# Kernel optimization log

Measured on AMD Instinct MI355X. Metric: run time of the kernel, lower is better.

Reference implementation:

```python
import jax, jax.numpy as jnp
import numpy as np

N0, N1, N2 = 200_000, 100_000, 80_000
F = 32
K5, K3 = 125, 27
M1, M2, M3, M4 = 20_000, 20_000, 30_000, 20_000
EPS = 1e-5


def sparse_conv(feats, W, in_idx, out_idx, n_out):
    """Gather-GEMM-scatter sparse conv. feats:[Nin,Cin], W:[K,Cin,Cout],
    in_idx/out_idx:[K,M] kernel map. Returns [n_out, Cout]."""
    g = feats[in_idx]                                  # [K, M, Cin] gather
    contrib = jnp.einsum('kmc,kcd->kmd', g, W)         # per-offset GEMM
    cout = W.shape[-1]
    out = jnp.zeros((n_out, cout), feats.dtype)
    return out.at[out_idx.reshape(-1)].add(contrib.reshape(-1, cout))


def bn(x, g, b):
    m = x.mean(0)
    v = x.var(0)
    return (x - m) * jax.lax.rsqrt(v + EPS) * g + b


def setup_inputs():
    key = jax.random.key(0)
    ks = jax.random.split(key, 16)
    W_SCALE = 0.02
    inp = {
        'x_feats': jax.random.normal(ks[0], (N0, 1), jnp.float32),
        'w1a': jax.random.normal(ks[1], (K5, 1, F), jnp.float32) * W_SCALE,
        'w1b': jax.random.normal(ks[2], (K5, F, F), jnp.float32) * W_SCALE,
        'w1c': jax.random.normal(ks[3], (K5, F, F), jnp.float32) * W_SCALE,
        'w2': jax.random.normal(ks[4], (K3, F, 2 * F), jnp.float32) * W_SCALE,
        'w3a': jax.random.normal(ks[5], (K3, 2 * F, 4 * F), jnp.float32) * W_SCALE,
        'w3b': jax.random.normal(ks[6], (K3, 4 * F, 8 * F), jnp.float32) * W_SCALE,
        'bn1b_g': jnp.ones((F,), jnp.float32), 'bn1b_b': jnp.zeros((F,), jnp.float32),
        'bn1c_g': jnp.ones((F,), jnp.float32), 'bn1c_b': jnp.zeros((F,), jnp.float32),
        'bn3a_g': jnp.ones((4 * F,), jnp.float32), 'bn3a_b': jnp.zeros((4 * F,), jnp.float32),
        'bn3b_g': jnp.ones((8 * F,), jnp.float32), 'bn3b_b': jnp.zeros((8 * F,), jnp.float32),
        'km1a_in': jax.random.randint(ks[7], (K5, M1), 0, N0, jnp.int32),
        'km1a_out': jax.random.randint(ks[8], (K5, M1), 0, N1, jnp.int32),
        'km1b_in': jax.random.randint(ks[9], (K5, M2), 0, N1, jnp.int32),
        'km1b_out': jax.random.randint(ks[10], (K5, M2), 0, N1, jnp.int32),
        'km1c_in': jax.random.randint(ks[11], (K5, M2), 0, N1, jnp.int32),
        'km1c_out': jax.random.randint(ks[12], (K5, M2), 0, N1, jnp.int32),
        'km2_in': jax.random.randint(ks[13], (K3, M3), 0, N1, jnp.int32),
        'km2_out': jax.random.randint(ks[14], (K3, M3), 0, N2, jnp.int32),
        'km3a_in': jax.random.randint(jax.random.fold_in(key, 20), (K3, M4), 0, N2, jnp.int32),
        'km3a_out': jax.random.randint(jax.random.fold_in(key, 21), (K3, M4), 0, N2, jnp.int32),
        'km3b_in': jax.random.randint(jax.random.fold_in(key, 22), (K3, M4), 0, N2, jnp.int32),
        'km3b_out': jax.random.randint(jax.random.fold_in(key, 23), (K3, M4), 0, N2, jnp.int32),
        'n1': N1,
        'n2': N2,
    }
    return inp


def reference(x_feats, w1a, w1b, w1c, w2, w3a, w3b,
              bn1b_g, bn1b_b, bn1c_g, bn1c_b, bn3a_g, bn3a_b, bn3b_g, bn3b_b,
              km1a_in, km1a_out, km1b_in, km1b_out, km1c_in, km1c_out,
              km2_in, km2_out, km3a_in, km3a_out, km3b_in, km3b_out, n1, n2):
    # enc1: conv(1->F, k5, s2) + ReLU
    h = jax.nn.relu(sparse_conv(x_feats, w1a, km1a_in, km1a_out, n1))
    # conv(F->F, k5) + BN + ReLU
    h = jax.nn.relu(bn(sparse_conv(h, w1b, km1b_in, km1b_out, n1), bn1b_g, bn1b_b))
    # conv(F->F, k5) + BN + ReLU
    x_e1 = jax.nn.relu(bn(sparse_conv(h, w1c, km1c_in, km1c_out, n1), bn1c_g, bn1c_b))
    # conv2: conv(F->2F, k3) onto c_out coordinates (no activation)
    h2 = sparse_conv(x_e1, w2, km2_in, km2_out, n2)
    # enc2: conv(2F->4F, k3) + BN + ReLU
    h2 = jax.nn.relu(bn(sparse_conv(h2, w3a, km3a_in, km3a_out, n2), bn3a_g, bn3a_b))
    # conv(4F->8F, k3) + BN + ReLU
    x_e2 = jax.nn.relu(bn(sparse_conv(h2, w3b, km3b_in, km3b_out, n2), bn3b_g, bn3b_b))
    return (x_e1, x_e2)
```

## Files before the change

### kernel.cpp

```cpp
#include <hip/hip_runtime.h>
#include <hip/hip_fp16.h>
#include <cstdint>
#include <algorithm>

#define N1c 100000
#define N2c 80000
#define EPSc 1e-5f
#define STRIDE_N1 102400
#define STRIDE_N2 81920

typedef _Float16 fp16x8 __attribute__((ext_vector_type(8)));
typedef float f32x4 __attribute__((ext_vector_type(4)));

__global__ __launch_bounds__(256) void rank2d_kernel(
    const int* __restrict__ out_idx, int* __restrict__ rank,
    int* __restrict__ bins, int E, int M, int q, int stride)
{
    for (int e = blockIdx.x * 256 + threadIdx.x; e < E; e += gridDim.x * 256) {
        int chunk = (e / M) / q;
        rank[e] = atomicAdd(&bins[chunk * stride + out_idx[e]], 1);
    }
}

__global__ __launch_bounds__(256) void scan1(
    const int* __restrict__ bins, int* __restrict__ ptr,
    int* __restrict__ bsums, int n)
{
    __shared__ int lds[256];
    int base = blockIdx.x * 1024;
    int v[4]; int t = 0;
    #pragma unroll
    for (int i = 0; i < 4; ++i) {
        int idx = base + threadIdx.x * 4 + i;
        v[i] = idx < n ? bins[idx] : 0;
        t += v[i];
    }
    lds[threadIdx.x] = t; __syncthreads();
    for (int off = 1; off < 256; off <<= 1) {
        int x = threadIdx.x >= off ? lds[threadIdx.x - off] : 0;
        __syncthreads();
        lds[threadIdx.x] += x;
        __syncthreads();
    }
    int run = lds[threadIdx.x] - t;
    if (threadIdx.x == 255) bsums[blockIdx.x] = lds[255];
    #pragma unroll
    for (int i = 0; i < 4; ++i) {
        int idx = base + threadIdx.x * 4 + i;
        if (idx < n) ptr[idx] = run;
        run += v[i];
    }
}

__global__ __launch_bounds__(64) void scan2s(
    int* __restrict__ bsums, int bpc, int nch)
{
    int c = threadIdx.x;
    if (c < nch) {
        int run = 0;
        for (int i = 0; i < bpc; ++i) {
            int idx = c * bpc + i;
            int t = bsums[idx]; bsums[idx] = run; run += t;
        }
    }
}

__global__ __launch_bounds__(256) void scan3(
    int* __restrict__ ptr, const int* __restrict__ bsums, int n)
{
    int idx = blockIdx.x * 1024 + threadIdx.x * 4;
    int add = bsums[blockIdx.x];
    #pragma unroll
    for (int i = 0; i < 4; ++i)
        if (idx + i < n) ptr[idx + i] += add;
}

__global__ __launch_bounds__(256) void scatter_1a(
    const float* __restrict__ x, const int* __restrict__ iin,
    const int* __restrict__ iout, const int* __restrict__ ptr,
    const int* __restrict__ rank, float2* __restrict__ payload, int E, int M)
{
    for (int e = blockIdx.x * 256 + threadIdx.x; e < E; e += gridDim.x * 256) {
        int k = e / M;
        float2 p; p.x = x[iin[e]]; p.y = __int_as_float(k);
        payload[ptr[iout[e]] + rank[e]] = p;
    }
}

__global__ __launch_bounds__(256) void phaseB_1a(
    const float2* __restrict__ payload, const int* __restrict__ ptr,
    const float* __restrict__ W, float* __restrict__ out, int n)
{
    __shared__ float Wl[125 * 32];
    for (int i = threadIdx.x; i < 125 * 32; i += 256) Wl[i] = W[i];
    __syncthreads();
    int total = n * 32;
    for (int idx = blockIdx.x * 256 + threadIdx.x; idx < total; idx += gridDim.x * 256) {
        int o = idx >> 5, c = idx & 31;
        int s0 = ptr[o], s1 = ptr[o + 1];
        float acc = 0.f;
        for (int s = s0; s < s1; ++s) {
            float2 p = payload[s];
            acc = fmaf(p.x, Wl[(__float_as_int(p.y) << 5) + c], acc);
        }
        out[idx] = fmaxf(acc, 0.f);
    }
}

template <int CIN, int CTILE, int WST, int GMODE>
__global__ __launch_bounds__(256) void phaseA_mfma(
    const float* __restrict__ feats, const float* __restrict__ W,
    const int* __restrict__ in_idx, const int* __restrict__ out_idx,
    const int* __restrict__ ptr, const int* __restrict__ rank,
    __half* __restrict__ contrib, int M,
    const float* __restrict__ sc, const float* __restrict__ sh)
{
    constexpr int PP  = 128;
    constexpr int NK  = CIN / 32;
    constexpr int NCF = CTILE / 16;
    constexpr int NRF = 2;
    constexpr int GCHK = (CIN * 2) / 16;
    constexpr int GSM  = (GCHK < 8 ? GCHK : 8) - 1;
    static_assert(CIN % 32 == 0 && CTILE % 16 == 0, "");

    __shared__ __align__(16) _Float16 Gl[PP * CIN];
    __shared__ __align__(16) _Float16 Wt[CTILE * CIN];
    __shared__ int sslot[PP];

    const int tid  = threadIdx.x;
    const int wave = tid >> 6;
    const int lane = tid & 63;
    const int k    = blockIdx.y;

    const int* iin  = in_idx  + (size_t)k * M;
    const int* iout = out_idx + (size_t)k * M;
    const int* rk   = rank    + (size_t)k * M;
    const float* Wk = W + (size_t)k * CIN * WST;

    for (int base = blockIdx.x * PP; base < M; base += gridDim.x * PP) {
        if (tid < PP && base + tid < M)
            sslot[tid] = ptr[iout[base + tid]] + rk[base + tid];

        {
            int r  = tid & (PP - 1);
            int hh = tid >> 7;
            int p  = base + r;
            if (p < M) {
                const int c0 = hh * (CIN / 2);
                const float* fr = feats + (size_t)iin[p] * CIN + c0;
                #pragma unroll
                for (int c = 0; c < CIN / 2; c += 8) {
                    float a[8];
                    *(float4*)&a[0] = *(const float4*)(fr + c);
                    *(float4*)&a[4] = *(const float4*)(fr + c + 4);
                    if (GMODE == 2) {
                        float s[8], h[8];
                        *(float4*)&s[0] = *(const float4*)(sc + c0 + c);
                        *(float4*)&s[4] = *(const float4*)(sc + c0 + c + 4);
                        *(float4*)&h[0] = *(const float4*)(sh + c0 + c);
                        *(float4*)&h[4] = *(const float4*)(sh + c0 + c + 4);
                        #pragma unroll
                        for (int j = 0; j < 8; ++j)
                            a[j] = fmaxf(fmaf(a[j], s[j], h[j]), 0.f);
                    }
                    _Float16 t[8];
                    #pragma unroll
                    for (int j = 0; j < 8; ++j) t[j] = (_Float16)a[j];
                    int col = c0 + c;
                    int idx = r * CIN + ((((col >> 3) ^ (r & GSM))) << 3);
                    *(uint4*)&Gl[idx] = *(uint4*)t;
                }
            }
        }

        for (int i = tid; i < (CTILE / 4) * (CIN / 4); i += 256) {
            int c4 = (i % (CTILE / 4)) * 4;
            int k4 = (i / (CTILE / 4)) * 4;
            const float* wr = Wk + (size_t)k4 * WST + c4;
            float a0[4], a1[4], a2[4], a3[4];
            *(float4*)a0 = *(const float4*)wr;
            *(float4*)a1 = *(const float4*)(wr + WST);
            *(float4*)a2 = *(const float4*)(wr + 2 * (size_t)WST);
            *(float4*)a3 = *(const float4*)(wr + 3 * (size_t)WST);
            #pragma unroll
            for (int j = 0; j < 4; ++j) {
                _Float16 t[4] = { (_Float16)a0[j], (_Float16)a1[j],
                                  (_Float16)a2[j], (_Float16)a3[j] };
                int row = c4 + j;
                int idx = row * CIN + (((k4 >> 3) ^ (row & GSM)) << 3) + (k4 & 7);
                *(uint2*)&Wt[idx] = *(uint2*)t;
            }
        }
        __syncthreads();

        f32x4 acc[NRF][NCF];
        #pragma unroll
        for (int rf = 0; rf < NRF; ++rf)
            #pragma unroll
            for (int cf = 0; cf < NCF; ++cf)
                acc[rf][cf] = (f32x4){0.f, 0.f, 0.f, 0.f};

        const int lrow = lane & 15;
        const int lk8  = (lane >> 4) * 8;
        const int p0   = wave * 32;
        #pragma unroll
        for (int kk = 0; kk < NK; ++kk) {
            int col = kk * 32 + lk8;
            fp16x8 afr[NRF];
            #pragma unroll
            for (int rf = 0; rf < NRF; ++rf) {
                int r = p0 + rf * 16 + lrow;
                afr[rf] = *(const fp16x8*)
                    &Gl[r * CIN + (((col >> 3) ^ (r & GSM)) << 3)];
            }
            #pragma unroll
            for (int cf = 0; cf < NCF; ++cf) {
                int r = cf * 16 + lrow;
                fp16x8 bfr = *(const fp16x8*)
                    &Wt[r * CIN + (((col >> 3) ^ (r & GSM)) << 3)];
                #pragma unroll
                for (int rf = 0; rf < NRF; ++rf)
                    acc[rf][cf] = __builtin_amdgcn_mfma_f32_16x16x32_f16(
                        afr[rf], bfr, acc[rf][cf], 0, 0, 0);
            }
        }

        #pragma unroll
        for (int rf = 0; rf < NRF; ++rf) {
            int prb = p0 + rf * 16 + (lane >> 4) * 4;
            #pragma unroll
            for (int b = 0; b < 4; ++b) {
                int pr = prb + b;
                if (base + pr < M) {
                    size_t s = (size_t)sslot[pr];
                    #pragma unroll
                    for (int cf = 0; cf < NCF; ++cf)
                        contrib[s * CTILE + cf * 16 + lrow] =
                            __float2half(acc[rf][cf][b]);
                }
            }
        }
        __syncthreads();
    }
}

template <int CSTR, bool STATS>
__global__ __launch_bounds__(256) void phaseB8(
    const __half* __restrict__ contrib, const int* __restrict__ ptr,
    float* __restrict__ out, int n, int ostr, int accum,
    double* __restrict__ statsbuf, int sqoff)
{
    float s1 = 0.f, s2 = 0.f;
    int total = n * CSTR;
    for (int idx = blockIdx.x * 256 + threadIdx.x; idx < total; idx += gridDim.x * 256) {
        int o = idx / CSTR, c = idx % CSTR;
        int a = ptr[o], b = ptr[o + 1];
        float acc = accum ? out[(size_t)o * ostr + c] : 0.f;
        for (int s = a; s < b; ++s)
            acc += __half2float(contrib[(size_t)s * CSTR + c]);
        out[(size_t)o * ostr + c] = acc;
        if (STATS) { s1 += acc; s2 += acc * acc; }
    }
    if constexpr (STATS) {
        __shared__ double l1[256], l2[256];
        l1[threadIdx.x] = (double)s1; l2[threadIdx.x] = (double)s2;
        __syncthreads();
        for (int off = 128; off >= CSTR; off >>= 1) {
            if (threadIdx.x < (unsigned)off) {
                l1[threadIdx.x] += l1[threadIdx.x + off];
                l2[threadIdx.x] += l2[threadIdx.x + off];
            }
            __syncthreads();
        }
        if (threadIdx.x < CSTR) {
            atomicAdd(&statsbuf[threadIdx.x], l1[threadIdx.x]);
            atomicAdd(&statsbuf[sqoff + threadIdx.x], l2[threadIdx.x]);
        }
    }
}

template <int C>
__global__ __launch_bounds__(256) void make_scsh(
    const double* __restrict__ sums, const float* __restrict__ g,
    const float* __restrict__ b, float* __restrict__ sc, float* __restrict__ sh,
    double inv_n)
{
    int c = threadIdx.x;
    if (c < C) {
        double mean = sums[c] * inv_n;
        double var  = sums[C + c] * inv_n - mean * mean;
        float s = g[c] * (float)(1.0 / sqrt(var + (double)EPSc));
        sc[c] = s;
        sh[c] = b[c] - (float)mean * s;
    }
}

template <int C>
__global__ __launch_bounds__(256) void bn_apply_relu_kernel(
    float* __restrict__ x, int n, const double* __restrict__ sums,
    const float* __restrict__ g, const float* __restrict__ b)
{
    const int c = threadIdx.x % C;
    const double inv_n = 1.0 / (double)n;
    double mean = sums[c] * inv_n;
    double var  = sums[C + c] * inv_n - mean * mean;
    float scale = g[c] * (float)(1.0 / sqrt(var + (double)EPSc));
    float shift = b[c] - (float)mean * scale;
    size_t total = (size_t)n * C;
    size_t stride = (size_t)gridDim.x * 256;
    for (size_t i = (size_t)blockIdx.x * 256 + threadIdx.x; i < total; i += stride)
        x[i] = fmaxf(x[i] * scale + shift, 0.f);
}

struct Plan { int q, nch; };

static Plan make_plan(long long tot_elems, int K, long long cap, int maxch)
{
    if (cap < 1) cap = 1;
    long long nch0 = (tot_elems + cap - 1) / cap;
    if (nch0 < 1) nch0 = 1;
    if (nch0 > K) nch0 = K;
    int q = (int)((K + nch0 - 1) / nch0);
    int nch = (K + q - 1) / q;
    if (nch > maxch) { q = (K + maxch - 1) / maxch; nch = (K + q - 1) / q; }
    return { q, nch };
}

static void build_csr2d(const int* iout, int* rank, int* bins, int* ptr, int* bsums,
                        int E, int M, int q, int nch, int stride, hipStream_t s)
{
    hipMemsetAsync(bins, 0, (size_t)nch * stride * sizeof(int), s);
    int gb = std::min(2048, (E + 255) / 256);
    hipLaunchKernelGGL(rank2d_kernel, dim3(gb), dim3(256), 0, s, iout, rank, bins, E, M, q, stride);
    int totalbins = nch * stride, nb = totalbins / 1024, bpc = stride / 1024;
    hipLaunchKernelGGL(scan1, dim3(nb), dim3(256), 0, s, bins, ptr, bsums, totalbins);
    hipLaunchKernelGGL(scan2s, dim3(1), dim3(64), 0, s, bsums, bpc, nch);
    hipLaunchKernelGGL(scan3, dim3(nb), dim3(256), 0, s, ptr, bsums, totalbins);
}

template <int CIN, int COUT, int GMODE, bool STATS>
static void run_layer(const float* feats, const float* W,
                      const int* iin, const int* iout, float* outp,
                      int M, int K, int n_out, int stride, int maxch,
                      int* bins, int* ptr, int* bsums, int* rank, __half* contrib,
                      long long cap_f32, const float* sc, const float* sh,
                      double* statsbuf, hipStream_t s)
{
    long long cap_h = cap_f32 * 2;
    Plan pl = make_plan((long long)K * M * COUT, K, cap_h, maxch);
    build_csr2d(iout, rank, bins, ptr, bsums, K * M, M, pl.q, pl.nch, stride, s);
    for (int ch = 0; ch < pl.nch; ++ch) {
        int k0 = ch * pl.q;
        int qc = std::min(pl.q, K - k0);
        dim3 g((M + 127) / 128, qc);
        hipLaunchKernelGGL((phaseA_mfma<CIN, COUT, COUT, GMODE>), g, dim3(256), 0, s,
                           feats, W + (size_t)k0 * CIN * COUT,
                           iin + (size_t)k0 * M, iout + (size_t)k0 * M,
                           ptr + (size_t)ch * stride, rank + (size_t)k0 * M,
                           contrib, M, sc, sh);
        bool last = (ch == pl.nch - 1);
        if (STATS && last)
            hipLaunchKernelGGL((phaseB8<COUT, true>), dim3(2048), dim3(256), 0, s,
                               contrib, ptr + (size_t)ch * stride, outp, n_out, COUT,
                               ch ? 1 : 0, statsbuf, COUT);
        else
            hipLaunchKernelGGL((phaseB8<COUT, false>), dim3(2048), dim3(256), 0, s,
                               contrib, ptr + (size_t)ch * stride, outp, n_out, COUT,
                               ch ? 1 : 0, (double*)nullptr, 0);
    }
}

extern "C" void kernel_launch(void* const* d_in, const int* in_sizes, int n_in,
                              void* d_out, int out_size, void* d_ws, size_t ws_size,
                              hipStream_t stream)
{
    const float* x_feats = (const float*)d_in[0];
    const float* w1a = (const float*)d_in[1];
    const float* w1b = (const float*)d_in[2];
    const float* w1c = (const float*)d_in[3];
    const float* w2  = (const float*)d_in[4];
    const float* w3a = (const float*)d_in[5];
    const float* w3b = (const float*)d_in[6];
    const float* bn1b_g = (const float*)d_in[7];
    const float* bn1b_b = (const float*)d_in[8];
    const float* bn1c_g = (const float*)d_in[9];
    const float* bn1c_b = (const float*)d_in[10];
    const float* bn3a_g = (const float*)d_in[11];
    const float* bn3a_b = (const float*)d_in[12];
    const float* bn3b_g = (const float*)d_in[13];
    const float* bn3b_b = (const float*)d_in[14];
    const int* km1a_in  = (const int*)d_in[15];
    const int* km1a_out = (const int*)d_in[16];
    const int* km1b_in  = (const int*)d_in[17];
    const int* km1b_out = (const int*)d_in[18];
    const int* km1c_in  = (const int*)d_in[19];
    const int* km1c_out = (const int*)d_in[20];
    const int* km2_in   = (const int*)d_in[21];
    const int* km2_out  = (const int*)d_in[22];
    const int* km3a_in  = (const int*)d_in[23];
    const int* km3a_out = (const int*)d_in[24];
    const int* km3b_in  = (const int*)d_in[25];
    const int* km3b_out = (const int*)d_in[26];

    float* out  = (float*)d_out;
    float* x_e1 = out;
    float* x_e2 = out + (size_t)N1c * 32;

    float* ws = (float*)d_ws;
    float*  poolA  = ws;
    float*  poolB  = poolA + 10240000;
    double* dstats = (double*)(poolB + 5120000);
    float*  scsh   = (float*)(dstats + 2048);
    int*    bins   = (int*)(scsh + 1024);
    int*    ptr    = bins + 819200;
    int*    bsums  = ptr + 819200;
    int*    rank   = bsums + 1024;
    float*  contribf = (float*)(rank + 2500000);
    __half* contrib  = (__half*)contribf;
    const long long FIXED = 10240000LL + 5120000 + 4096 + 1024
                          + 819200 + 819200 + 1024 + 2500000;
    long long cap = (long long)(ws_size / 4) - FIXED - 32;
    if (cap < 1) cap = 1;

    float* h1  = poolA;
    float* h3  = poolA;
    float* h2  = poolB;
    float* h2b = poolB;

    double* dst1b = dstats;
    double* dst1c = dstats + 512;
    double* dst3a = dstats + 1024;
    double* dst3b = dstats + 1536;
    float* sc1b = scsh,       *sh1b = scsh + 32;
    float* sc3a = scsh + 256, *sh3a = scsh + 384;

    hipMemsetAsync(dstats, 0, 2048 * sizeof(double), stream);

    {
        build_csr2d(km1a_out, rank, bins, ptr, bsums, 125 * 20000, 20000, 125, 1,
                    STRIDE_N1, stream);
        hipLaunchKernelGGL(scatter_1a, dim3(2048), dim3(256), 0, stream,
                           x_feats, km1a_in, km1a_out, ptr, rank, (float2*)contribf,
                           125 * 20000, 20000);
        hipLaunchKernelGGL(phaseB_1a, dim3(2048), dim3(256), 0, stream,
                           (const float2*)contribf, ptr, w1a, h1, N1c);
    }

    run_layer<32, 32, 0, true>(h1, w1b, km1b_in, km1b_out, h2, 20000, 125, N1c,
                               STRIDE_N1, 8, bins, ptr, bsums, rank, contrib,
                               cap, nullptr, nullptr, dst1b, stream);
    hipLaunchKernelGGL((make_scsh<32>), dim3(1), dim3(256), 0, stream,
                       dst1b, bn1b_g, bn1b_b, sc1b, sh1b, 1.0 / N1c);

    run_layer<32, 32, 2, true>(h2, w1c, km1c_in, km1c_out, x_e1, 20000, 125, N1c,
                               STRIDE_N1, 8, bins, ptr, bsums, rank, contrib,
                               cap, sc1b, sh1b, dst1c, stream);
    hipLaunchKernelGGL((bn_apply_relu_kernel<32>), dim3(2048), dim3(256), 0, stream,
                       x_e1, N1c, dst1c, bn1c_g, bn1c_b);

    run_layer<32, 64, 0, false>(x_e1, w2, km2_in, km2_out, h2b, 30000, 27, N2c,
                                STRIDE_N2, 10, bins, ptr, bsums, rank, contrib,
                                cap, nullptr, nullptr, nullptr, stream);

    run_layer<64, 128, 0, true>(h2b, w3a, km3a_in, km3a_out, h3, 20000, 27, N2c,
                                STRIDE_N2, 10, bins, ptr, bsums, rank, contrib,
                                cap, nullptr, nullptr, dst3a, stream);
    hipLaunchKernelGGL((make_scsh<128>), dim3(1), dim3(256), 0, stream,
                       dst3a, bn3a_g, bn3a_b, sc3a, sh3a, 1.0 / N2c);

    {
        const int M = 20000, K = 27;
        Plan pl = make_plan((long long)K * M * 128, K, cap * 2, 10);
        build_csr2d(km3b_out, rank, bins, ptr, bsums, K * M, M, pl.q, pl.nch,
                    STRIDE_N2, stream);
        for (int half = 0; half < 2; ++half) {
            for (int ch = 0; ch < pl.nch; ++ch) {
                int k0 = ch * pl.q;
                int qc = std::min(pl.q, K - k0);
                dim3 g((20000 + 127) / 128, qc);
                hipLaunchKernelGGL((phaseA_mfma<128, 128, 256, 2>), g, dim3(256), 0, stream,
                                   h3, w3b + half * 128 + (size_t)k0 * 128 * 256,
                                   km3b_in + (size_t)k0 * M, km3b_out + (size_t)k0 * M,
                                   ptr + (size_t)ch * STRIDE_N2, rank + (size_t)k0 * M,
                                   contrib, M, sc3a, sh3a);
                bool last = (ch == pl.nch - 1);
                if (last)
                    hipLaunchKernelGGL((phaseB8<128, true>), dim3(2048), dim3(256), 0, stream,
                                       contrib, ptr + (size_t)ch * STRIDE_N2,
                                       x_e2 + half * 128, N2c, 256, ch ? 1 : 0,
                                       dst3b + half * 128, 256);
                else
                    hipLaunchKernelGGL((phaseB8<128, false>), dim3(2048), dim3(256), 0, stream,
                                       contrib, ptr + (size_t)ch * STRIDE_N2,
                                       x_e2 + half * 128, N2c, 256, ch ? 1 : 0,
                                       (double*)nullptr, 0);
            }
        }
        hipLaunchKernelGGL((bn_apply_relu_kernel<256>), dim3(2048), dim3(256), 0, stream,
                           x_e2, N2c, dst3b, bn3b_g, bn3b_b);
    }
}
```

Measured before the change: 1.989 ms.

## Store intermediate activations in fp16 and pre-convert weights to fp16 once per layer

Intermediate feature maps (h1, h2, h2b, h3) are now kept in fp16 instead of fp32, which halves the bytes moved by the gathers in phaseA and by the read-modify-write in phaseB. Weights are converted to an fp16 [K][COUT][CIN] layout by a separate kernel per layer. phaseA then reads its B fragments straight from global memory instead of staging a transposed weight tile in shared memory, which cuts LDS use and lets the launch bounds request 3 blocks per SM. The costs are extra rounding of intermediates to fp16 and B-fragment loads from global/L2 with no reuse through LDS.

```diff
diff --git a/kernel.cpp b/kernel.cpp
--- a/kernel.cpp
+++ b/kernel.cpp
@@ -75,6 +75,19 @@
         if (idx + i < n) ptr[idx + i] += add;
 }
 
+__global__ __launch_bounds__(256) void wconv_fp16(
+    const float* __restrict__ W, _Float16* __restrict__ Wh,
+    int K, int CIN, int CTILE, int WST, int total)
+{
+    for (int idx = blockIdx.x * 256 + threadIdx.x; idx < total;
+         idx += gridDim.x * 256) {
+        int k = idx / (CTILE * CIN);
+        int c = (idx / CIN) % CTILE;
+        int j = idx % CIN;
+        Wh[idx] = (_Float16)W[(size_t)k * CIN * WST + (size_t)j * WST + c];
+    }
+}
+
 __global__ __launch_bounds__(256) void scatter_1a(
     const float* __restrict__ x, const int* __restrict__ iin,
     const int* __restrict__ iout, const int* __restrict__ ptr,
@@ -89,7 +102,7 @@
 
 __global__ __launch_bounds__(256) void phaseB_1a(
     const float2* __restrict__ payload, const int* __restrict__ ptr,
-    const float* __restrict__ W, float* __restrict__ out, int n)
+    const float* __restrict__ W, __half* __restrict__ out, int n)
 {
     __shared__ float Wl[125 * 32];
     for (int i = threadIdx.x; i < 125 * 32; i += 256) Wl[i] = W[i];
@@ -103,13 +116,13 @@
             float2 p = payload[s];
             acc = fmaf(p.x, Wl[(__float_as_int(p.y) << 5) + c], acc);
         }
-        out[idx] = fmaxf(acc, 0.f);
-    }
-}
-
-template <int CIN, int CTILE, int WST, int GMODE>
-__global__ __launch_bounds__(256) void phaseA_mfma(
-    const float* __restrict__ feats, const float* __restrict__ W,
+        out[idx] = __float2half(fmaxf(acc, 0.f));
+    }
+}
+
+template <int CIN, int CTILE, int GMODE, int IN16>
+__global__ __launch_bounds__(256, 3) void phaseA_mfma(
+    const void* __restrict__ feats_, const _Float16* __restrict__ Wh,
     const int* __restrict__ in_idx, const int* __restrict__ out_idx,
     const int* __restrict__ ptr, const int* __restrict__ rank,
     __half* __restrict__ contrib, int M,
@@ -119,12 +132,11 @@
     constexpr int NK  = CIN / 32;
     constexpr int NCF = CTILE / 16;
     constexpr int NRF = 2;
-    constexpr int GCHK = (CIN * 2) / 16;
-    constexpr int GSM  = (GCHK < 8 ? GCHK : 8) - 1;
+    constexpr int GCHK = CIN / 8;
+    constexpr int GSM  = (GCHK < 16 ? GCHK : 16) - 1;
     static_assert(CIN % 32 == 0 && CTILE % 16 == 0, "");
 
     __shared__ __align__(16) _Float16 Gl[PP * CIN];
-    __shared__ __align__(16) _Float16 Wt[CTILE * CIN];
     __shared__ int sslot[PP];
 
     const int tid  = threadIdx.x;
@@ -135,7 +147,7 @@
     const int* iin  = in_idx  + (size_t)k * M;
     const int* iout = out_idx + (size_t)k * M;
     const int* rk   = rank    + (size_t)k * M;
-    const float* Wk = W + (size_t)k * CIN * WST;
+    const _Float16* Wk = Wh + (size_t)k * CTILE * CIN;
 
     for (int base = blockIdx.x * PP; base < M; base += gridDim.x * PP) {
         if (tid < PP && base + tid < M)
@@ -147,48 +159,46 @@
             int p  = base + r;
             if (p < M) {
                 const int c0 = hh * (CIN / 2);
-                const float* fr = feats + (size_t)iin[p] * CIN + c0;
-                #pragma unroll
-                for (int c = 0; c < CIN / 2; c += 8) {
-                    float a[8];
-                    *(float4*)&a[0] = *(const float4*)(fr + c);
-                    *(float4*)&a[4] = *(const float4*)(fr + c + 4);
-                    if (GMODE == 2) {
-                        float s[8], h[8];
-                        *(float4*)&s[0] = *(const float4*)(sc + c0 + c);
-                        *(float4*)&s[4] = *(const float4*)(sc + c0 + c + 4);
-                        *(float4*)&h[0] = *(const float4*)(sh + c0 + c);
-                        *(float4*)&h[4] = *(const float4*)(sh + c0 + c + 4);
+                if (IN16) {
+                    const _Float16* fr =
+                        (const _Float16*)feats_ + (size_t)iin[p] * CIN + c0;
+                    #pragma unroll
+                    for (int c = 0; c < CIN / 2; c += 8) {
+                        fp16x8 v = *(const fp16x8*)(fr + c);
+                        if (GMODE == 2) {
+                            #pragma unroll
+                            for (int j = 0; j < 8; ++j) {
+                                float x = fmaf((float)v[j], sc[c0 + c + j],
+                                               sh[c0 + c + j]);
+                                v[j] = (_Float16)fmaxf(x, 0.f);
+                            }
+                        }
+                        int col = c0 + c;
+                        int idx = r * CIN + (((col >> 3) ^ (r & GSM)) << 3);
+                        *(fp16x8*)&Gl[idx] = v;
+                    }
+                } else {
+                    const float* fr =
+                        (const float*)feats_ + (size_t)iin[p] * CIN + c0;
+                    #pragma unroll
+                    for (int c = 0; c < CIN / 2; c += 8) {
+                        float a[8];
+                        *(float4*)&a[0] = *(const float4*)(fr + c);
+                        *(float4*)&a[4] = *(const float4*)(fr + c + 4);
+                        if (GMODE == 2) {
+                            #pragma unroll
+                            for (int j = 0; j < 8; ++j)
+                                a[j] = fmaxf(fmaf(a[j], sc[c0 + c + j],
+                                                  sh[c0 + c + j]), 0.f);
+                        }
+                        fp16x8 v;
                         #pragma unroll
-                        for (int j = 0; j < 8; ++j)
-                            a[j] = fmaxf(fmaf(a[j], s[j], h[j]), 0.f);
+                        for (int j = 0; j < 8; ++j) v[j] = (_Float16)a[j];
+                        int col = c0 + c;
+                        int idx = r * CIN + (((col >> 3) ^ (r & GSM)) << 3);
+                        *(fp16x8*)&Gl[idx] = v;
                     }
-                    _Float16 t[8];
-                    #pragma unroll
-                    for (int j = 0; j < 8; ++j) t[j] = (_Float16)a[j];
-                    int col = c0 + c;
-                    int idx = r * CIN + ((((col >> 3) ^ (r & GSM))) << 3);
-                    *(uint4*)&Gl[idx] = *(uint4*)t;
                 }
-            }
-        }
-
-        for (int i = tid; i < (CTILE / 4) * (CIN / 4); i += 256) {
-            int c4 = (i % (CTILE / 4)) * 4;
-            int k4 = (i / (CTILE / 4)) * 4;
-            const float* wr = Wk + (size_t)k4 * WST + c4;
-            float a0[4], a1[4], a2[4], a3[4];
-            *(float4*)a0 = *(const float4*)wr;
-            *(float4*)a1 = *(const float4*)(wr + WST);
-            *(float4*)a2 = *(const float4*)(wr + 2 * (size_t)WST);
-            *(float4*)a3 = *(const float4*)(wr + 3 * (size_t)WST);
-            #pragma unroll
-            for (int j = 0; j < 4; ++j) {
-                _Float16 t[4] = { (_Float16)a0[j], (_Float16)a1[j],
-                                  (_Float16)a2[j], (_Float16)a3[j] };
-                int row = c4 + j;
-                int idx = row * CIN + (((k4 >> 3) ^ (row & GSM)) << 3) + (k4 & 7);
-                *(uint2*)&Wt[idx] = *(uint2*)t;
             }
         }
         __syncthreads();
@@ -215,9 +225,8 @@
             }
             #pragma unroll
             for (int cf = 0; cf < NCF; ++cf) {
-                int r = cf * 16 + lrow;
                 fp16x8 bfr = *(const fp16x8*)
-                    &Wt[r * CIN + (((col >> 3) ^ (r & GSM)) << 3)];
+                    &Wk[(size_t)(cf * 16 + lrow) * CIN + col];
                 #pragma unroll
                 for (int rf = 0; rf < NRF; ++rf)
                     acc[rf][cf] = __builtin_amdgcn_mfma_f32_16x16x32_f16(
@@ -244,10 +253,10 @@
     }
 }
 
-template <int CSTR, bool STATS>
+template <int CSTR, bool STATS, int OUT16>
 __global__ __launch_bounds__(256) void phaseB8(
     const __half* __restrict__ contrib, const int* __restrict__ ptr,
-    float* __restrict__ out, int n, int ostr, int accum,
+    void* __restrict__ out_, int n, int ostr, int accum,
     double* __restrict__ statsbuf, int sqoff)
 {
     float s1 = 0.f, s2 = 0.f;
@@ -255,10 +264,16 @@
     for (int idx = blockIdx.x * 256 + threadIdx.x; idx < total; idx += gridDim.x * 256) {
         int o = idx / CSTR, c = idx % CSTR;
         int a = ptr[o], b = ptr[o + 1];
-        float acc = accum ? out[(size_t)o * ostr + c] : 0.f;
+        size_t oi = (size_t)o * ostr + c;
+        float acc;
+        if (OUT16)
+            acc = accum ? __half2float(((const __half*)out_)[oi]) : 0.f;
+        else
+            acc = accum ? ((const float*)out_)[oi] : 0.f;
         for (int s = a; s < b; ++s)
             acc += __half2float(contrib[(size_t)s * CSTR + c]);
-        out[(size_t)o * ostr + c] = acc;
+        if (OUT16) ((__half*)out_)[oi] = __float2half(acc);
+        else       ((float*)out_)[oi] = acc;
         if (STATS) { s1 += acc; s2 += acc * acc; }
     }
     if constexpr (STATS) {
@@ -338,14 +353,18 @@
     hipLaunchKernelGGL(scan3, dim3(nb), dim3(256), 0, s, ptr, bsums, totalbins);
 }
 
-template <int CIN, int COUT, int GMODE, bool STATS>
-static void run_layer(const float* feats, const float* W,
-                      const int* iin, const int* iout, float* outp,
+template <int CIN, int COUT, int GMODE, bool STATS, int IN16, int OUT16>
+static void run_layer(const void* feats, const float* W,
+                      const int* iin, const int* iout, void* outp,
                       int M, int K, int n_out, int stride, int maxch,
                       int* bins, int* ptr, int* bsums, int* rank, __half* contrib,
-                      long long cap_f32, const float* sc, const float* sh,
+                      _Float16* wh, long long cap_f32,
+                      const float* sc, const float* sh,
                       double* statsbuf, hipStream_t s)
 {
+    int wtot = K * COUT * CIN;
+    hipLaunchKernelGGL(wconv_fp16, dim3(std::min(2048, (wtot + 255) / 256)),
+                       dim3(256), 0, s, W, wh, K, CIN, COUT, COUT, wtot);
     long long cap_h = cap_f32 * 2;
     Plan pl = make_plan((long long)K * M * COUT, K, cap_h, maxch);
     build_csr2d(iout, rank, bins, ptr, bsums, K * M, M, pl.q, pl.nch, stride, s);
@@ -353,18 +372,18 @@
         int k0 = ch * pl.q;
         int qc = std::min(pl.q, K - k0);
         dim3 g((M + 127) / 128, qc);
-        hipLaunchKernelGGL((phaseA_mfma<CIN, COUT, COUT, GMODE>), g, dim3(256), 0, s,
-                           feats, W + (size_t)k0 * CIN * COUT,
+        hipLaunchKernelGGL((phaseA_mfma<CIN, COUT, GMODE, IN16>), g, dim3(256), 0, s,
+                           feats, wh + (size_t)k0 * COUT * CIN,
                            iin + (size_t)k0 * M, iout + (size_t)k0 * M,
                            ptr + (size_t)ch * stride, rank + (size_t)k0 * M,
                            contrib, M, sc, sh);
         bool last = (ch == pl.nch - 1);
         if (STATS && last)
-            hipLaunchKernelGGL((phaseB8<COUT, true>), dim3(2048), dim3(256), 0, s,
+            hipLaunchKernelGGL((phaseB8<COUT, true, OUT16>), dim3(2048), dim3(256), 0, s,
                                contrib, ptr + (size_t)ch * stride, outp, n_out, COUT,
                                ch ? 1 : 0, statsbuf, COUT);
         else
-            hipLaunchKernelGGL((phaseB8<COUT, false>), dim3(2048), dim3(256), 0, s,
+            hipLaunchKernelGGL((phaseB8<COUT, false, OUT16>), dim3(2048), dim3(256), 0, s,
                                contrib, ptr + (size_t)ch * stride, outp, n_out, COUT,
                                ch ? 1 : 0, (double*)nullptr, 0);
     }
@@ -415,17 +434,19 @@
     int*    ptr    = bins + 819200;
     int*    bsums  = ptr + 819200;
     int*    rank   = bsums + 1024;
-    float*  contribf = (float*)(rank + 2500000);
+    float*  whf    = (float*)(rank + 2500000);
+    _Float16* wh   = (_Float16*)whf;
+    float*  contribf = whf + 221200;
     __half* contrib  = (__half*)contribf;
     const long long FIXED = 10240000LL + 5120000 + 4096 + 1024
-                          + 819200 + 819200 + 1024 + 2500000;
+                          + 819200 + 819200 + 1024 + 2500000 + 221200;
     long long cap = (long long)(ws_size / 4) - FIXED - 32;
     if (cap < 1) cap = 1;
 
-    float* h1  = poolA;
-    float* h3  = poolA;
-    float* h2  = poolB;
-    float* h2b = poolB;
+    __half* h1  = (__half*)poolA;
+    __half* h3  = (__half*)poolA;
+    __half* h2  = (__half*)poolB;
+    __half* h2b = (__half*)poolB;
 
     double* dst1b = dstats;
     double* dst1c = dstats + 512;
@@ -446,25 +467,25 @@
                            (const float2*)contribf, ptr, w1a, h1, N1c);
     }
 
-    run_layer<32, 32, 0, true>(h1, w1b, km1b_in, km1b_out, h2, 20000, 125, N1c,
-                               STRIDE_N1, 8, bins, ptr, bsums, rank, contrib,
-                               cap, nullptr, nullptr, dst1b, stream);
+    run_layer<32, 32, 0, true, 1, 1>(h1, w1b, km1b_in, km1b_out, h2, 20000, 125, N1c,
+                                     STRIDE_N1, 8, bins, ptr, bsums, rank, contrib,
+                                     wh, cap, nullptr, nullptr, dst1b, stream);
     hipLaunchKernelGGL((make_scsh<32>), dim3(1), dim3(256), 0, stream,
                        dst1b, bn1b_g, bn1b_b, sc1b, sh1b, 1.0 / N1c);
 
-    run_layer<32, 32, 2, true>(h2, w1c, km1c_in, km1c_out, x_e1, 20000, 125, N1c,
-                               STRIDE_N1, 8, bins, ptr, bsums, rank, contrib,
-                               cap, sc1b, sh1b, dst1c, stream);
+    run_layer<32, 32, 2, true, 1, 0>(h2, w1c, km1c_in, km1c_out, x_e1, 20000, 125, N1c,
+                                     STRIDE_N1, 8, bins, ptr, bsums, rank, contrib,
+                                     wh, cap, sc1b, sh1b, dst1c, stream);
     hipLaunchKernelGGL((bn_apply_relu_kernel<32>), dim3(2048), dim3(256), 0, stream,
                        x_e1, N1c, dst1c, bn1c_g, bn1c_b);
 
-    run_layer<32, 64, 0, false>(x_e1, w2, km2_in, km2_out, h2b, 30000, 27, N2c,
-                                STRIDE_N2, 10, bins, ptr, bsums, rank, contrib,
-                                cap, nullptr, nullptr, nullptr, stream);
-
-    run_layer<64, 128, 0, true>(h2b, w3a, km3a_in, km3a_out, h3, 20000, 27, N2c,
-                                STRIDE_N2, 10, bins, ptr, bsums, rank, contrib,
-                                cap, nullptr, nullptr, dst3a, stream);
+    run_layer<32, 64, 0, false, 0, 1>(x_e1, w2, km2_in, km2_out, h2b, 30000, 27, N2c,
+                                      STRIDE_N2, 10, bins, ptr, bsums, rank, contrib,
+                                      wh, cap, nullptr, nullptr, nullptr, stream);
+
+    run_layer<64, 128, 0, true, 1, 1>(h2b, w3a, km3a_in, km3a_out, h3, 20000, 27, N2c,
+                                      STRIDE_N2, 10, bins, ptr, bsums, rank, contrib,
+                                      wh, cap, nullptr, nullptr, dst3a, stream);
     hipLaunchKernelGGL((make_scsh<128>), dim3(1), dim3(256), 0, stream,
                        dst3a, bn3a_g, bn3a_b, sc3a, sh3a, 1.0 / N2c);
 
@@ -474,23 +495,26 @@
         build_csr2d(km3b_out, rank, bins, ptr, bsums, K * M, M, pl.q, pl.nch,
                     STRIDE_N2, stream);
         for (int half = 0; half < 2; ++half) {
+            int wtot = K * 128 * 128;
+            hipLaunchKernelGGL(wconv_fp16, dim3(2048), dim3(256), 0, stream,
+                               w3b + half * 128, wh, K, 128, 128, 256, wtot);
             for (int ch = 0; ch < pl.nch; ++ch) {
                 int k0 = ch * pl.q;
                 int qc = std::min(pl.q, K - k0);
                 dim3 g((20000 + 127) / 128, qc);
-                hipLaunchKernelGGL((phaseA_mfma<128, 128, 256, 2>), g, dim3(256), 0, stream,
-                                   h3, w3b + half * 128 + (size_t)k0 * 128 * 256,
+                hipLaunchKernelGGL((phaseA_mfma<128, 128, 2, 1>), g, dim3(256), 0, stream,
+                                   h3, wh + (size_t)k0 * 128 * 128,
                                    km3b_in + (size_t)k0 * M, km3b_out + (size_t)k0 * M,
                                    ptr + (size_t)ch * STRIDE_N2, rank + (size_t)k0 * M,
                                    contrib, M, sc3a, sh3a);
                 bool last = (ch == pl.nch - 1);
                 if (last)
-                    hipLaunchKernelGGL((phaseB8<128, true>), dim3(2048), dim3(256), 0, stream,
+                    hipLaunchKernelGGL((phaseB8<128, true, 0>), dim3(2048), dim3(256), 0, stream,
                                        contrib, ptr + (size_t)ch * STRIDE_N2,
                                        x_e2 + half * 128, N2c, 256, ch ? 1 : 0,
                                        dst3b + half * 128, 256);
                 else
-                    hipLaunchKernelGGL((phaseB8<128, false>), dim3(2048), dim3(256), 0, stream,
+                    hipLaunchKernelGGL((phaseB8<128, false, 0>), dim3(2048), dim3(256), 0, stream,
                                        contrib, ptr + (size_t)ch * STRIDE_N2,
                                        x_e2 + half * 128, N2c, 256, ch ? 1 : 0,
                                        (double*)nullptr, 0);
```

After: 2.239 ms. +12.6%, slower.
